# Kernel optimization log

Measured on AMD Instinct MI355X. Metric: run time of the kernel, lower is better.

The kernel has to match this reference:

```python
import jax, jax.numpy as jnp
import numpy as np

T, B, D, H, Q = 512, 256, 128, 128, 8


def _qgate(z, theta):
    """Analytic simulation of the QGate circuit.

    Circuit: start |0..0>, RX(z_j) then trainable RX(theta_j) on each wire j
    (RX(a)RX(b)=RX(a+b)), then a CNOT ring w->(w+1)%Q, then <Z_w> on each wire.
    RX(phi)|0> gives <Z>=cos(phi) and independent wires; the CNOT ring permutes
    computational basis states so bit_w = XOR_{j<=w} a_j for w>=1 and
    bit_0 = XOR_{j>=1} a_j, hence <Z_w> = prod_{j<=w} cos(phi_j) for w>=1 and
    <Z_0> = prod_{j>=1} cos(phi_j). Exact, no 2^Q statevector needed.
    """
    c = jnp.cos(z + theta)                      # (B, Q)
    cp = jnp.cumprod(c, axis=-1)                # (B, Q)
    z0 = jnp.prod(c[:, 1:], axis=-1, keepdims=True)
    return jnp.concatenate([z0, cp[:, 1:]], axis=-1)


def setup_inputs() -> dict:
    key = jax.random.key(0)
    ks = jax.random.split(key, 25)
    inp = {"inputs": jax.random.normal(ks[0], (T, B, D), dtype=jnp.float32)}
    s_in = 1.0 / np.sqrt(D + H)
    s_q = 1.0 / np.sqrt(Q)
    names = ["f", "i", "g", "o"]
    for n, gname in enumerate(names):
        k = ks[1 + 6 * n: 1 + 6 * (n + 1)]
        inp["W" + gname] = jax.random.uniform(k[0], (Q, D + H), jnp.float32, -s_in, s_in)
        inp["b" + gname] = jax.random.uniform(k[1], (Q,), jnp.float32, -s_in, s_in)
        inp["th" + gname] = jax.random.normal(k[2], (Q,), jnp.float32)  # trainable RX angles
        inp["U" + gname] = jax.random.uniform(k[3], (H, Q), jnp.float32, -s_q, s_q)
        inp["c" + gname] = jax.random.uniform(k[4], (H,), jnp.float32, -s_q, s_q)
    return inp


def reference(inputs, Wf, bf, thf, Uf, cf,
              Wi, bi, thi, Ui, ci,
              Wg, bg, thg, Ug, cg,
              Wo, bo, tho, Uo, co):
    bsz = inputs.shape[1]
    hdim = Uf.shape[0]
    h0 = jnp.zeros((bsz, hdim), inputs.dtype)
    c0 = jnp.zeros((bsz, hdim), inputs.dtype)

    def gate(comb, W, b, th, U, cb):
        return _qgate(comb @ W.T + b, th) @ U.T + cb

    def step(carry, x):
        hx, cx = carry
        comb = jnp.concatenate([x, hx], axis=1)          # (B, D+H)
        f = jax.nn.sigmoid(gate(comb, Wf, bf, thf, Uf, cf))
        i = jax.nn.sigmoid(gate(comb, Wi, bi, thi, Ui, ci))
        g = jnp.tanh(gate(comb, Wg, bg, thg, Ug, cg))
        o = jax.nn.sigmoid(gate(comb, Wo, bo, tho, Uo, co))
        cx = f * cx + i * g
        hx = o * jnp.tanh(cx)
        return (hx, cx), hx

    (hx, cx), outs = jax.lax.scan(step, (h0, c0), inputs)
    return outs, hx, cx
```

## Files before the change

### kernel.cpp

```cpp
#include <hip/hip_runtime.h>

#define TT 512
#define BB 256
#define DD 128
#define HH 128
#define QQ 8

struct Params {
    const float* x;
    const float* W[4];
    const float* b[4];
    const float* th[4];
    const float* U[4];
    const float* cb[4];
    float* out;
};

__device__ __forceinline__ float rcp_f(float x)  { return __builtin_amdgcn_rcpf(x); }
__device__ __forceinline__ float exp2_f(float x) { return __builtin_amdgcn_exp2f(x); }

template<int CTRL>
__device__ __forceinline__ float dpp_mov(float x) {
    int r = __builtin_amdgcn_update_dpp(0, __float_as_int(x), CTRL, 0xF, 0xF, true);
    return __int_as_float(r);
}
template<int CTRL, int RM>
__device__ __forceinline__ float dpp_mul1(float x) {
    int r = __builtin_amdgcn_update_dpp(0x3f800000 , __float_as_int(x),
                                        CTRL, RM, 0xF, false);
    return __int_as_float(r);
}
#define RDLANE(v, l) __int_as_float(__builtin_amdgcn_readlane(__float_as_int(v), (l)))

__device__ __forceinline__ void bar_lds() {
    asm volatile("s_waitcnt lgkmcnt(0)\n\ts_barrier" ::: "memory");
}

__global__ __launch_bounds__(256, 1) void qlstm(Params p) {
    __shared__ __align__(16) float xbuf[2][8][144];
    __shared__ __align__(16) float hbuf[144];
    __shared__ float pre[512];
    __shared__ float zxbuf[2][32];

    const int tid = threadIdx.x;
    const int bId = blockIdx.x;
    const int ln  = tid & 63;
    const int wv  = tid >> 6;
    const int qub = ln >> 3;
    const int part8 = ln & 7;

    float Wh[16];
    {
        const float* Wg = p.W[wv] + qub * (DD + HH) + DD + part8 * 16;
        #pragma unroll
        for (int j = 0; j < 16; ++j) Wh[j] = Wg[j];
    }
    const float breg = p.b[wv][qub] + p.th[wv][qub];

    const int gz = 2 * (wv - 2) + (ln >> 5);
    const int qz = (ln >> 2) & 7;
    const int pz = ln & 3;
    float Wx[32];
    if (wv >= 2) {
        const float* Wg = p.W[gz] + qz * (DD + HH) + pz * 32;
        #pragma unroll
        for (int j = 0; j < 32; ++j) Wx[j] = Wg[j];
    }

    const float esc = (wv == 2) ? 2.885390081777927f : -1.442695040888963f;
    float Ua[8], Ub[8];
    #pragma unroll
    for (int j = 0; j < 8; ++j) {
        Ua[j] = p.U[wv][ln * QQ + j] * esc;
        Ub[j] = p.U[wv][(ln + 64) * QQ + j] * esc;
    }
    const float cba = p.cb[wv][ln] * esc;
    const float cbb = p.cb[wv][ln + 64] * esc;

    float cst = 0.f;
    float hn_last = 0.f;

    if (tid < 128) hbuf[tid + 4 * (tid >> 5)] = 0.f;

    const int xc_col  = (ln & 31) * 4;
    const int xc_half = ln >> 5;
    const int xc_slot = xc_col + 4 * (xc_col >> 5);
    float4 xr[4];
    #pragma unroll
    for (int j = 0; j < 4; ++j) xr[j] = make_float4(0.f, 0.f, 0.f, 0.f);

    if (wv == 3) {
        #pragma unroll
        for (int j = 0; j < 4; ++j) {
            const int row = 2 * j + xc_half;
            float4 v = *(const float4*)(p.x + ((size_t)row * BB + bId) * DD + xc_col);
            *(float4*)&xbuf[0][row][xc_slot] = v;
        }
    }
    __syncthreads();

    if (wv >= 2) {
        const float* xrow = &xbuf[0][0][36 * pz];
        float b0 = 0.f, b1 = 0.f, b2 = 0.f, b3 = 0.f;
        #pragma unroll
        for (int i = 0; i < 8; ++i) {
            float4 c4 = *(const float4*)(xrow + 4 * i);
            b0 = fmaf(Wx[4*i+0], c4.x, b0);
            b1 = fmaf(Wx[4*i+1], c4.y, b1);
            b2 = fmaf(Wx[4*i+2], c4.z, b2);
            b3 = fmaf(Wx[4*i+3], c4.w, b3);
        }
        float zx2 = (b0 + b1) + (b2 + b3);
        zx2 += dpp_mov<0xB1>(zx2);
        zx2 += dpp_mov<0x4E>(zx2);
        if ((ln & 3) == 0) zxbuf[0][8 * gz + qz] = zx2;
    }
    __syncthreads();

    #pragma unroll 8
    for (int t = 0; t < TT; ++t) {
        if (((t & 7) == 0) && wv == 3) {
            const int tch = (t >> 3) + 1;
            if (tch < TT / 8) {
                #pragma unroll
                for (int j = 0; j < 4; ++j) {
                    const int row = tch * 8 + 2 * j + xc_half;
                    xr[j] = *(const float4*)(p.x + ((size_t)row * BB + bId) * DD + xc_col);
                }
            }
        }

        const float zxs = zxbuf[t & 1][8 * wv + qub];
        const float* hsrc = &hbuf[16 * part8 + 4 * (part8 >> 1)];
        float a0 = 0.f, a1 = 0.f, a2 = 0.f, a3 = 0.f;
        #pragma unroll
        for (int i = 0; i < 4; ++i) {
            float4 c4 = *(const float4*)(hsrc + 4 * i);
            a0 = fmaf(Wh[4*i+0], c4.x, a0);
            a1 = fmaf(Wh[4*i+1], c4.y, a1);
            a2 = fmaf(Wh[4*i+2], c4.z, a2);
            a3 = fmaf(Wh[4*i+3], c4.w, a3);
        }
        float acc = (a0 + a1) + (a2 + a3);
        acc += dpp_mov<0xB1>(acc);
        acc += dpp_mov<0x4E>(acc);
        acc += dpp_mov<0x141>(acc);
        acc += zxs + breg;

        const float cv = __cosf(acc);
        float v = cv;
        v *= dpp_mul1<0x118, 0xF>(v);
        v *= dpp_mul1<0x142, 0xA>(v);
        v *= dpp_mul1<0x143, 0xC>(v);
        float u = (ln < 8) ? 1.f : cv;
        u *= dpp_mul1<0x118, 0xF>(u);
        u *= dpp_mul1<0x142, 0xA>(u);
        u *= dpp_mul1<0x143, 0xC>(u);
        const float q0 = RDLANE(u, 63);
        const float q1 = RDLANE(v, 8);
        const float q2 = RDLANE(v, 16);
        const float q3 = RDLANE(v, 24);
        const float q4 = RDLANE(v, 32);
        const float q5 = RDLANE(v, 40);
        const float q6 = RDLANE(v, 48);
        const float q7 = RDLANE(v, 56);

        float pa = fmaf(Ua[0], q0, cba); float pb = fmaf(Ub[0], q0, cbb);
        pa = fmaf(Ua[1], q1, pa);        pb = fmaf(Ub[1], q1, pb);
        pa = fmaf(Ua[2], q2, pa);        pb = fmaf(Ub[2], q2, pb);
        pa = fmaf(Ua[3], q3, pa);        pb = fmaf(Ub[3], q3, pb);
        pa = fmaf(Ua[4], q4, pa);        pb = fmaf(Ub[4], q4, pb);
        pa = fmaf(Ua[5], q5, pa);        pb = fmaf(Ub[5], q5, pb);
        pa = fmaf(Ua[6], q6, pa);        pb = fmaf(Ub[6], q6, pb);
        pa = fmaf(Ua[7], q7, pa);        pb = fmaf(Ub[7], q7, pb);
        pre[wv * 128 + ln]      = pa;
        pre[wv * 128 + 64 + ln] = pb;

        bar_lds();

        if (tid < 128) {
            float p_f = (wv == 0) ? pa : pre[tid];
            float p_i = (wv == 1) ? pb : pre[128 + tid];
            float p_g = pre[256 + tid];
            float p_o = pre[384 + tid];
            float fg = rcp_f(1.f + exp2_f(p_f));
            float ig = rcp_f(1.f + exp2_f(p_i));
            float gg = 1.f - 2.f * rcp_f(1.f + exp2_f(p_g));
            float og = rcp_f(1.f + exp2_f(p_o));
            cst = fmaf(fg, cst, ig * gg);
            float tc = 1.f - 2.f * rcp_f(1.f + exp2_f(cst * 2.885390081777927f));
            float hn = og * tc;
            hn_last = hn;
            hbuf[tid + 4 * (tid >> 5)] = hn;
            p.out[(size_t)(t * BB + bId) * HH + tid] = hn;
        } else {
            if (wv == 3 && (t & 7) == 6) {
                const int tch = (t >> 3) + 1;
                if (tch < TT / 8) {
                    #pragma unroll
                    for (int j = 0; j < 4; ++j) {
                        const int row = 2 * j + xc_half;
                        *(float4*)&xbuf[tch & 1][row][xc_slot] = xr[j];
                    }
                }
            }
            if (t < TT - 1) {
                const int tn = t + 1;
                const float* xrow = &xbuf[(tn >> 3) & 1][tn & 7][36 * pz];
                float b0 = 0.f, b1 = 0.f, b2 = 0.f, b3 = 0.f;
                #pragma unroll
                for (int i = 0; i < 8; ++i) {
                    float4 c4 = *(const float4*)(xrow + 4 * i);
                    b0 = fmaf(Wx[4*i+0], c4.x, b0);
                    b1 = fmaf(Wx[4*i+1], c4.y, b1);
                    b2 = fmaf(Wx[4*i+2], c4.z, b2);
                    b3 = fmaf(Wx[4*i+3], c4.w, b3);
                }
                float zx2 = (b0 + b1) + (b2 + b3);
                zx2 += dpp_mov<0xB1>(zx2);
                zx2 += dpp_mov<0x4E>(zx2);
                if ((ln & 3) == 0) zxbuf[tn & 1][8 * gz + qz] = zx2;
            }
        }
        bar_lds();
    }

    if (tid < 128) {
        p.out[(size_t)TT * BB * HH + (size_t)bId * HH + tid] = hn_last;
        p.out[(size_t)TT * BB * HH + (size_t)BB * HH + (size_t)bId * HH + tid] = cst;
    }
}

extern "C" void kernel_launch(void* const* d_in, const int* in_sizes, int n_in,
                              void* d_out, int out_size, void* d_ws, size_t ws_size,
                              hipStream_t stream) {
    (void)in_sizes; (void)n_in; (void)out_size; (void)d_ws; (void)ws_size;
    Params p;
    p.x = (const float*)d_in[0];
    for (int g = 0; g < 4; ++g) {
        p.W[g]  = (const float*)d_in[1 + 5 * g + 0];
        p.b[g]  = (const float*)d_in[1 + 5 * g + 1];
        p.th[g] = (const float*)d_in[1 + 5 * g + 2];
        p.U[g]  = (const float*)d_in[1 + 5 * g + 3];
        p.cb[g] = (const float*)d_in[1 + 5 * g + 4];
    }
    p.out = (float*)d_out;
    hipLaunchKernelGGL(qlstm, dim3(BB), dim3(256), 0, stream, p);
}
```

Baseline: 372.3 us.

## Replicate LSTM cell update in every wave to drop second barrier per step

Each of the four waves now redundantly computes the full 128-wide cell/hidden update from double-buffered gate pre-activations and keeps its own private copy of h in LDS. This removes the second block barrier per timestep. The x-projection is also redistributed so each wave computes its own gate's input term locally, with no shared zx buffer. The trade is four times the transcendental work for the cell update and more per-wave x-projection FMAs, in exchange for one fewer barrier on the serial critical path.

```diff
diff --git a/kernel.cpp b/kernel.cpp
--- a/kernel.cpp
+++ b/kernel.cpp
@@ -38,9 +38,8 @@
 
 __global__ __launch_bounds__(256, 1) void qlstm(Params p) {
     __shared__ __align__(16) float xbuf[2][8][144];
-    __shared__ __align__(16) float hbuf[144];
-    __shared__ float pre[512];
-    __shared__ float zxbuf[2][32];
+    __shared__ __align__(16) float hb[4][144];
+    __shared__ __align__(16) float pre[2][4][128];
 
     const int tid = threadIdx.x;
     const int bId = blockIdx.x;
@@ -49,23 +48,15 @@
     const int qub = ln >> 3;
     const int part8 = ln & 7;
 
-    float Wh[16];
+    float Wh[16], Wx[16];
     {
-        const float* Wg = p.W[wv] + qub * (DD + HH) + DD + part8 * 16;
-        #pragma unroll
-        for (int j = 0; j < 16; ++j) Wh[j] = Wg[j];
+        const float* Wg = p.W[wv] + qub * (DD + HH);
+        #pragma unroll
+        for (int j = 0; j < 16; ++j) Wx[j] = Wg[part8 * 16 + j];
+        #pragma unroll
+        for (int j = 0; j < 16; ++j) Wh[j] = Wg[DD + part8 * 16 + j];
     }
     const float breg = p.b[wv][qub] + p.th[wv][qub];
-
-    const int gz = 2 * (wv - 2) + (ln >> 5);
-    const int qz = (ln >> 2) & 7;
-    const int pz = ln & 3;
-    float Wx[32];
-    if (wv >= 2) {
-        const float* Wg = p.W[gz] + qz * (DD + HH) + pz * 32;
-        #pragma unroll
-        for (int j = 0; j < 32; ++j) Wx[j] = Wg[j];
-    }
 
     const float esc = (wv == 2) ? 2.885390081777927f : -1.442695040888963f;
     float Ua[8], Ub[8];
@@ -77,61 +68,55 @@
     const float cba = p.cb[wv][ln] * esc;
     const float cbb = p.cb[wv][ln + 64] * esc;
 
-    float cst = 0.f;
-    float hn_last = 0.f;
-
-    if (tid < 128) hbuf[tid + 4 * (tid >> 5)] = 0.f;
-
-    const int xc_col  = (ln & 31) * 4;
-    const int xc_half = ln >> 5;
-    const int xc_slot = xc_col + 4 * (xc_col >> 5);
-    float4 xr[4];
-    #pragma unroll
-    for (int j = 0; j < 4; ++j) xr[j] = make_float4(0.f, 0.f, 0.f, 0.f);
-
-    if (wv == 3) {
-        #pragma unroll
-        for (int j = 0; j < 4; ++j) {
-            const int row = 2 * j + xc_half;
-            float4 v = *(const float4*)(p.x + ((size_t)row * BB + bId) * DD + xc_col);
-            *(float4*)&xbuf[0][row][xc_slot] = v;
-        }
-    }
-    __syncthreads();
-
-    if (wv >= 2) {
-        const float* xrow = &xbuf[0][0][36 * pz];
+    const int sa = ln + 4 * (ln >> 5);
+    const int sb = sa + 72;
+    float csta = 0.f, cstb = 0.f, hna = 0.f, hnb = 0.f;
+    hb[wv][sa] = 0.f;
+    hb[wv][sb] = 0.f;
+
+    const int xrow_ = 2 * wv + (ln >> 5);
+    const int xcol  = (ln & 31) * 4;
+    const int xslot = xcol + 4 * (xcol >> 5);
+    {
+        float4 v0 = *(const float4*)(p.x + ((size_t)xrow_ * BB + bId) * DD + xcol);
+        *(float4*)&xbuf[0][xrow_][xslot] = v0;
+    }
+    bar_lds();
+
+    const int lsoff = 16 * part8 + 4 * (part8 >> 1);
+    const float* hsrc = &hb[wv][lsoff];
+
+    float zxc;
+    {
+        const float* xr0 = &xbuf[0][0][lsoff];
         float b0 = 0.f, b1 = 0.f, b2 = 0.f, b3 = 0.f;
         #pragma unroll
-        for (int i = 0; i < 8; ++i) {
-            float4 c4 = *(const float4*)(xrow + 4 * i);
+        for (int i = 0; i < 4; ++i) {
+            float4 c4 = *(const float4*)(xr0 + 4 * i);
             b0 = fmaf(Wx[4*i+0], c4.x, b0);
             b1 = fmaf(Wx[4*i+1], c4.y, b1);
             b2 = fmaf(Wx[4*i+2], c4.z, b2);
             b3 = fmaf(Wx[4*i+3], c4.w, b3);
         }
-        float zx2 = (b0 + b1) + (b2 + b3);
-        zx2 += dpp_mov<0xB1>(zx2);
-        zx2 += dpp_mov<0x4E>(zx2);
-        if ((ln & 3) == 0) zxbuf[0][8 * gz + qz] = zx2;
-    }
-    __syncthreads();
+        float z = (b0 + b1) + (b2 + b3);
+        z += dpp_mov<0xB1>(z);
+        z += dpp_mov<0x4E>(z);
+        z += dpp_mov<0x141>(z);
+        zxc = z;
+    }
+
+    float4 xr = make_float4(0.f, 0.f, 0.f, 0.f);
 
     #pragma unroll 8
     for (int t = 0; t < TT; ++t) {
-        if (((t & 7) == 0) && wv == 3) {
+        if ((t & 7) == 0) {
             const int tch = (t >> 3) + 1;
             if (tch < TT / 8) {
-                #pragma unroll
-                for (int j = 0; j < 4; ++j) {
-                    const int row = tch * 8 + 2 * j + xc_half;
-                    xr[j] = *(const float4*)(p.x + ((size_t)row * BB + bId) * DD + xc_col);
-                }
+                const int row = tch * 8 + xrow_;
+                xr = *(const float4*)(p.x + ((size_t)row * BB + bId) * DD + xcol);
             }
         }
 
-        const float zxs = zxbuf[t & 1][8 * wv + qub];
-        const float* hsrc = &hbuf[16 * part8 + 4 * (part8 >> 1)];
         float a0 = 0.f, a1 = 0.f, a2 = 0.f, a3 = 0.f;
         #pragma unroll
         for (int i = 0; i < 4; ++i) {
@@ -145,7 +130,7 @@
         acc += dpp_mov<0xB1>(acc);
         acc += dpp_mov<0x4E>(acc);
         acc += dpp_mov<0x141>(acc);
-        acc += zxs + breg;
+        acc += zxc + breg;
 
         const float cv = __cosf(acc);
         float v = cv;
@@ -173,61 +158,80 @@
         pa = fmaf(Ua[5], q5, pa);        pb = fmaf(Ub[5], q5, pb);
         pa = fmaf(Ua[6], q6, pa);        pb = fmaf(Ub[6], q6, pb);
         pa = fmaf(Ua[7], q7, pa);        pb = fmaf(Ub[7], q7, pb);
-        pre[wv * 128 + ln]      = pa;
-        pre[wv * 128 + 64 + ln] = pb;
+        pre[t & 1][wv][ln]      = pa;
+        pre[t & 1][wv][64 + ln] = pb;
+
+        if ((t & 7) == 6) {
+            const int tch = (t >> 3) + 1;
+            if (tch < TT / 8) {
+                *(float4*)&xbuf[tch & 1][xrow_][xslot] = xr;
+            }
+        }
 
         bar_lds();
 
-        if (tid < 128) {
-            float p_f = (wv == 0) ? pa : pre[tid];
-            float p_i = (wv == 1) ? pb : pre[128 + tid];
-            float p_g = pre[256 + tid];
-            float p_o = pre[384 + tid];
-            float fg = rcp_f(1.f + exp2_f(p_f));
-            float ig = rcp_f(1.f + exp2_f(p_i));
-            float gg = 1.f - 2.f * rcp_f(1.f + exp2_f(p_g));
-            float og = rcp_f(1.f + exp2_f(p_o));
-            cst = fmaf(fg, cst, ig * gg);
-            float tc = 1.f - 2.f * rcp_f(1.f + exp2_f(cst * 2.885390081777927f));
-            float hn = og * tc;
-            hn_last = hn;
-            hbuf[tid + 4 * (tid >> 5)] = hn;
-            p.out[(size_t)(t * BB + bId) * HH + tid] = hn;
-        } else {
-            if (wv == 3 && (t & 7) == 6) {
-                const int tch = (t >> 3) + 1;
-                if (tch < TT / 8) {
-                    #pragma unroll
-                    for (int j = 0; j < 4; ++j) {
-                        const int row = 2 * j + xc_half;
-                        *(float4*)&xbuf[tch & 1][row][xc_slot] = xr[j];
-                    }
-                }
+        const float pf_a = pre[t & 1][0][ln];
+        const float pi_a = pre[t & 1][1][ln];
+        const float pg_a = pre[t & 1][2][ln];
+        const float po_a = pre[t & 1][3][ln];
+        const float pf_b = pre[t & 1][0][64 + ln];
+        const float pi_b = pre[t & 1][1][64 + ln];
+        const float pg_b = pre[t & 1][2][64 + ln];
+        const float po_b = pre[t & 1][3][64 + ln];
+
+        float fga = rcp_f(1.f + exp2_f(pf_a));
+        float iga = rcp_f(1.f + exp2_f(pi_a));
+        float gga = 1.f - 2.f * rcp_f(1.f + exp2_f(pg_a));
+        float oga = rcp_f(1.f + exp2_f(po_a));
+        csta = fmaf(fga, csta, iga * gga);
+        const float tca = 1.f - 2.f * rcp_f(1.f + exp2_f(csta * 2.885390081777927f));
+        hna = oga * tca;
+
+        float fgb = rcp_f(1.f + exp2_f(pf_b));
+        float igb = rcp_f(1.f + exp2_f(pi_b));
+        float ggb = 1.f - 2.f * rcp_f(1.f + exp2_f(pg_b));
+        float ogb = rcp_f(1.f + exp2_f(po_b));
+        cstb = fmaf(fgb, cstb, igb * ggb);
+        const float tcb = 1.f - 2.f * rcp_f(1.f + exp2_f(cstb * 2.885390081777927f));
+        hnb = ogb * tcb;
+
+        hb[wv][sa] = hna;
+        hb[wv][sb] = hnb;
+
+        if (wv == 0) {
+            float* o = p.out + (size_t)(t * BB + bId) * HH;
+            o[ln]      = hna;
+            o[ln + 64] = hnb;
+        }
+
+        float zxn = 0.f;
+        if (t < TT - 1) {
+            const int tn = t + 1;
+            const float* xr0 = &xbuf[(tn >> 3) & 1][tn & 7][lsoff];
+            float b0 = 0.f, b1 = 0.f, b2 = 0.f, b3 = 0.f;
+            #pragma unroll
+            for (int i = 0; i < 4; ++i) {
+                float4 c4 = *(const float4*)(xr0 + 4 * i);
+                b0 = fmaf(Wx[4*i+0], c4.x, b0);
+                b1 = fmaf(Wx[4*i+1], c4.y, b1);
+                b2 = fmaf(Wx[4*i+2], c4.z, b2);
+                b3 = fmaf(Wx[4*i+3], c4.w, b3);
             }
-            if (t < TT - 1) {
-                const int tn = t + 1;
-                const float* xrow = &xbuf[(tn >> 3) & 1][tn & 7][36 * pz];
-                float b0 = 0.f, b1 = 0.f, b2 = 0.f, b3 = 0.f;
-                #pragma unroll
-                for (int i = 0; i < 8; ++i) {
-                    float4 c4 = *(const float4*)(xrow + 4 * i);
-                    b0 = fmaf(Wx[4*i+0], c4.x, b0);
-                    b1 = fmaf(Wx[4*i+1], c4.y, b1);
-                    b2 = fmaf(Wx[4*i+2], c4.z, b2);
-                    b3 = fmaf(Wx[4*i+3], c4.w, b3);
-                }
-                float zx2 = (b0 + b1) + (b2 + b3);
-                zx2 += dpp_mov<0xB1>(zx2);
-                zx2 += dpp_mov<0x4E>(zx2);
-                if ((ln & 3) == 0) zxbuf[tn & 1][8 * gz + qz] = zx2;
-            }
-        }
-        bar_lds();
-    }
-
-    if (tid < 128) {
-        p.out[(size_t)TT * BB * HH + (size_t)bId * HH + tid] = hn_last;
-        p.out[(size_t)TT * BB * HH + (size_t)BB * HH + (size_t)bId * HH + tid] = cst;
+            float z = (b0 + b1) + (b2 + b3);
+            z += dpp_mov<0xB1>(z);
+            z += dpp_mov<0x4E>(z);
+            z += dpp_mov<0x141>(z);
+            zxn = z;
+        }
+        zxc = zxn;
+    }
+
+    if (wv == 0) {
+        float* o = p.out + (size_t)TT * BB * HH;
+        o[(size_t)bId * HH + ln]             = hna;
+        o[(size_t)bId * HH + ln + 64]        = hnb;
+        o[(size_t)(BB + bId) * HH + ln]      = csta;
+        o[(size_t)(BB + bId) * HH + ln + 64] = cstb;
     }
 }
 
```

Measured after the change: 468.5 us. 25.8% more time.
